# Kernel optimization log

Measured on AMD Instinct MI355X. Metric: run time of the kernel, lower is better.

Reference implementation:

```python
import jax, jax.numpy as jnp
import numpy as np
from jax import lax

EPS = 1e-5


def _dcn_core(value, offset, mask, offset_scale):
    # value: (B,H,W,G,D); offset: (B,H,W,G,K,2) as (dx,dy); mask: (B,H,W,G,K)
    # DCNv4: no softmax on mask; sampling loc = center + (kernel_grid + offset)*offset_scale
    B, H, W, G, D = value.shape
    K = mask.shape[-1]
    P = H * W
    kr = jnp.arange(3, dtype=value.dtype) - 1.0
    gy, gx = jnp.meshgrid(kr, kr, indexing="ij")  # 3x3 kernel grid
    gx = gx.reshape(1, 1, 1, 1, K)
    gy = gy.reshape(1, 1, 1, 1, K)
    bx = jnp.arange(W, dtype=value.dtype).reshape(1, 1, W, 1, 1)
    by = jnp.arange(H, dtype=value.dtype).reshape(1, H, 1, 1, 1)
    ix = bx + (gx + offset[..., 0]) * offset_scale  # (B,H,W,G,K) pixel-index coords
    iy = by + (gy + offset[..., 1]) * offset_scale

    tog = lambda a: a.transpose(0, 3, 1, 2, 4).reshape(B, G, P, K)
    ix, iy, m = tog(ix), tog(iy), tog(mask)
    vflat = value.transpose(0, 3, 1, 2, 4).reshape(B, G, P, D)

    x0 = jnp.floor(ix)
    y0 = jnp.floor(iy)
    tx = ix - x0
    ty = iy - y0
    out = jnp.zeros((B, G, P, D), value.dtype)
    # bilinear with zero padding (grid_sample padding_mode='zeros', align_corners=False)
    for dy, dx, wgt in ((0, 0, (1 - ty) * (1 - tx)), (0, 1, (1 - ty) * tx),
                        (1, 0, ty * (1 - tx)), (1, 1, ty * tx)):
        xc = x0 + dx
        yc = y0 + dy
        valid = ((xc >= 0) & (xc < W) & (yc >= 0) & (yc < H)).astype(value.dtype)
        lin = (jnp.clip(yc, 0, H - 1) * W + jnp.clip(xc, 0, W - 1)).astype(jnp.int32)
        v = jnp.take_along_axis(vflat, lin.reshape(B, G, P * K, 1), axis=2)
        v = v.reshape(B, G, P, K, D)
        out = out + jnp.einsum("bgpk,bgpkd->bgpd", wgt * m * valid, v)
    return out.transpose(0, 2, 1, 3).reshape(B, P, G * D)


def setup_inputs() -> dict:
    key = jax.random.key(0)
    ks = jax.random.split(key, 6)
    C = 64
    r = lambda k, shp, s: jax.random.normal(k, shp, jnp.float32) * s
    return {
        "x": r(ks[0], (8, C, 128, 128), 1.0),
        "vp_w": r(ks[1], (C, C), C ** -0.5),
        "vp_b": jnp.zeros((C,), jnp.float32),
        "dw_w": r(ks[2], (C, 1, 3, 3), 1.0 / 3.0),
        "dw_b": jnp.zeros((C,), jnp.float32),
        "om_w": r(ks[3], (56, C), 0.01),
        "om_b": jnp.zeros((56,), jnp.float32),
        "op_w": r(ks[4], (C, C), C ** -0.5),
        "op_b": jnp.zeros((C,), jnp.float32),
        "bn_g": jnp.ones((C // 2,), jnp.float32),
        "bn_b": jnp.zeros((C // 2,), jnp.float32),
        "bn_m": jnp.zeros((C // 2,), jnp.float32),
        "bn_v": jnp.ones((C // 2,), jnp.float32),
    }


def reference(x, vp_w, vp_b, dw_w, dw_b, om_w, om_b, op_w, op_b, bn_g, bn_b, bn_m, bn_v):
    B, C, H, W = x.shape
    G, K, OS = 2, 9, 2.0  # group = in_planes//out_planes = 2; 3x3 -> K=9
    seq = x.reshape(B, H * W, C)  # raw reshape exactly as the torch code
    # DCNv4 value_proj
    val = seq @ vp_w.T + vp_b
    value = val.reshape(B, H, W, G, C // G)
    # offset/mask branch: depthwise 3x3 conv on raw input, then linear
    xi = seq.reshape(B, H, W, C).transpose(0, 3, 1, 2)  # (B,C,H,W)
    dw = lax.conv_general_dilated(xi, dw_w, (1, 1), "SAME",
                                  dimension_numbers=("NCHW", "OIHW", "NCHW"),
                                  feature_group_count=C)
    dw = dw + dw_b[None, :, None, None]
    om = dw.transpose(0, 2, 3, 1) @ om_w.T + om_b  # (B,H,W,56)
    om = om[..., : G * K * 3].reshape(B, H, W, G, 3 * K)  # drop pad-to-8 tail
    offset = om[..., : 2 * K].reshape(B, H, W, G, K, 2)
    mask = om[..., 2 * K:]
    core = _dcn_core(value, offset, mask, OS)  # (B, HW, C)
    out = (core @ op_w.T + op_b).reshape(B, C, H, W)  # raw reshape, as in torch code
    z = 0.5 * (out[:, : C // 2] + out[:, C // 2:])  # chunk + average
    z = bn_g[:, None, None] * (z - bn_m[:, None, None]) * lax.rsqrt(bn_v + EPS)[:, None, None] + bn_b[:, None, None]
    return jnp.maximum(z, 0.0)
```

## Files before the change

kernel.cpp:

```cpp
#include <hip/hip_runtime.h>

#define B_ 8
#define H_ 128
#define W_ 128
#define P_ 16384
#define C_ 64
#define NQ (B_*P_)

typedef _Float16 fp16;
typedef _Float16 half2v __attribute__((ext_vector_type(2)));
typedef _Float16 half4v __attribute__((ext_vector_type(4)));
typedef _Float16 half8v __attribute__((ext_vector_type(8)));

static __device__ __forceinline__ void fma4s(float4& a, float s, const float4& v) {
  a.x += s * v.x; a.y += s * v.y; a.z += s * v.z; a.w += s * v.w;
}
static __device__ __forceinline__ void fma4e(float4& a, const float4& u, const float4& v) {
  a.x += u.x * v.x; a.y += u.y * v.y; a.z += u.z * v.z; a.w += u.w * v.w;
}
static __device__ __forceinline__ float4 h2f(half4v h) {
  return make_float4((float)h.x, (float)h.y, (float)h.z, (float)h.w);
}
static __device__ __forceinline__ half4v f2h(float4 a) {
  half4v hv;
  hv.x = (fp16)a.x; hv.y = (fp16)a.y; hv.z = (fp16)a.z; hv.w = (fp16)a.w;
  return hv;
}

__global__ __launch_bounds__(256) void gemm_val_kernel(
    const float* __restrict__ X, const float* __restrict__ W,
    const float* __restrict__ bias, fp16* __restrict__ val) {
  __shared__ __align__(16) float Xs[128][68];
  __shared__ __align__(16) float Ws[64][68];
  int tid = threadIdx.x;
  int bid = blockIdx.x;
  int logical = (bid & 7) * 128 + (bid >> 3);
  size_t row0 = (size_t)logical * 128;

#pragma unroll
  for (int i0 = 0; i0 < 8192; i0 += 1024) {
    int i = i0 + tid * 4;
    int r = i >> 6, k = i & 63;
    *(float4*)&Xs[r][k] = *(const float4*)(X + row0 * 64 + i);
  }
#pragma unroll
  for (int i0 = 0; i0 < 4096; i0 += 1024) {
    int i = i0 + tid * 4;
    int c = i >> 6, k = i & 63;
    float4 wv = *(const float4*)(W + i);
    Ws[k][c] = wv.x; Ws[k + 1][c] = wv.y; Ws[k + 2][c] = wv.z; Ws[k + 3][c] = wv.w;
  }
  __syncthreads();

  int ty = tid >> 4, tx = tid & 15;
  int c0 = tx * 4;
  float4 b4 = *(const float4*)(bias + c0);
  float4 acc[8];
#pragma unroll
  for (int rr = 0; rr < 8; ++rr) acc[rr] = b4;
#pragma unroll 4
  for (int k0 = 0; k0 < 64; k0 += 4) {
    float4 w0 = *(const float4*)&Ws[k0][c0];
    float4 w1 = *(const float4*)&Ws[k0 + 1][c0];
    float4 w2 = *(const float4*)&Ws[k0 + 2][c0];
    float4 w3 = *(const float4*)&Ws[k0 + 3][c0];
#pragma unroll
    for (int rr = 0; rr < 8; ++rr) {
      float4 xv = *(const float4*)&Xs[ty + rr * 16][k0];
      fma4s(acc[rr], xv.x, w0); fma4s(acc[rr], xv.y, w1);
      fma4s(acc[rr], xv.z, w2); fma4s(acc[rr], xv.w, w3);
    }
  }
#pragma unroll
  for (int rr = 0; rr < 8; ++rr) {
    int r = ty + rr * 16;
    *(half4v*)(val + (row0 + r) * 64 + c0) = f2h(acc[rr]);
  }
}

__global__ __launch_bounds__(256) void dwom_kernel(
    const float* __restrict__ X, const float* __restrict__ dw_w,
    const float* __restrict__ dw_b, const float* __restrict__ om_w,
    const float* __restrict__ om_b, fp16* __restrict__ OM) {
  __shared__ __align__(16) fp16 dws[64][76];
  __shared__ __align__(16) fp16 omwT[64][60];
  __shared__ __align__(16) float dwwT[9][68];
  __shared__ float dwbs[64];
  __shared__ float ombs[56];
  int tid = threadIdx.x;
  int bid = blockIdx.x;
  int logical = (bid & 7) * 256 + (bid >> 3);
  int b = logical >> 8;
  int lg = logical & 255;
  int q0 = b * 16384 + lg * 64;
  int h = lg >> 1;
  int w0 = (lg & 1) * 64;

  for (int i = tid; i < 3456; i += 256) omwT[i & 63][i >> 6] = (fp16)om_w[i];
  for (int i = tid; i < 576; i += 256) dwwT[i % 9][i / 9] = dw_w[i];
  if (tid < 64) dwbs[tid] = dw_b[tid];
  if (tid < 56) ombs[tid] = (tid < 54) ? om_b[tid] : 0.f;
  __syncthreads();

  {
    int cv = tid & 15;
    int wq = tid >> 4;
    int c0 = cv * 4;
    int wbase = w0 + wq * 4;
    const float* xb = X + (size_t)b * 1048576 + c0;
    const float* rp0 = xb + (size_t)(h - 1) * 8192;
    const float* rp1 = xb + (size_t)h * 8192;
    const float* rp2 = xb + (size_t)(h + 1) * 8192;
    bool v0 = (h > 0), v2 = (h < 127);
    float4 wt[9];
#pragma unroll
    for (int t = 0; t < 9; ++t) wt[t] = *(const float4*)&dwwT[t][c0];
    float4 dwb4 = *(const float4*)&dwbs[c0];
    const float4 z4 = make_float4(0.f, 0.f, 0.f, 0.f);
    bool vm = (wbase > 0);
    float4 cm0 = (vm && v0) ? *(const float4*)(rp0 + (wbase - 1) * 64) : z4;
    float4 cm1 = vm         ? *(const float4*)(rp1 + (wbase - 1) * 64) : z4;
    float4 cm2 = (vm && v2) ? *(const float4*)(rp2 + (wbase - 1) * 64) : z4;
    float4 cc0 = v0 ? *(const float4*)(rp0 + wbase * 64) : z4;
    float4 cc1 =      *(const float4*)(rp1 + wbase * 64);
    float4 cc2 = v2 ? *(const float4*)(rp2 + wbase * 64) : z4;
#pragma unroll
    for (int j = 0; j < 4; ++j) {
      int w = wbase + j;
      bool vn = (w < 127);
      float4 cn0 = (vn && v0) ? *(const float4*)(rp0 + (w + 1) * 64) : z4;
      float4 cn1 = vn         ? *(const float4*)(rp1 + (w + 1) * 64) : z4;
      float4 cn2 = (vn && v2) ? *(const float4*)(rp2 + (w + 1) * 64) : z4;
      float4 acc = dwb4;
      fma4e(acc, cm0, wt[0]); fma4e(acc, cc0, wt[1]); fma4e(acc, cn0, wt[2]);
      fma4e(acc, cm1, wt[3]); fma4e(acc, cc1, wt[4]); fma4e(acc, cn1, wt[5]);
      fma4e(acc, cm2, wt[6]); fma4e(acc, cc2, wt[7]); fma4e(acc, cn2, wt[8]);
      *(half4v*)&dws[wq * 4 + j][c0] = f2h(acc);
      cm0 = cc0; cm1 = cc1; cm2 = cc2;
      cc0 = cn0; cc1 = cn1; cc2 = cn2;
    }
  }
  __syncthreads();

  int ty = tid >> 4, tx = tid & 15;
  int o0 = tx * 4;
  if (o0 < 54) {
    float4 b4 = *(const float4*)&ombs[o0];
    float4 acc[4] = {b4, b4, b4, b4};
#pragma unroll 4
    for (int k0 = 0; k0 < 64; k0 += 4) {
      float4 w0 = h2f(*(const half4v*)&omwT[k0][o0]);
      float4 w1 = h2f(*(const half4v*)&omwT[k0 + 1][o0]);
      float4 w2 = h2f(*(const half4v*)&omwT[k0 + 2][o0]);
      float4 w3 = h2f(*(const half4v*)&omwT[k0 + 3][o0]);
#pragma unroll
      for (int rr = 0; rr < 4; ++rr) {
        float4 dv = h2f(*(const half4v*)&dws[ty * 4 + rr][k0]);
        fma4s(acc[rr], dv.x, w0); fma4s(acc[rr], dv.y, w1);
        fma4s(acc[rr], dv.z, w2); fma4s(acc[rr], dv.w, w3);
      }
    }
#pragma unroll
    for (int rr = 0; rr < 4; ++rr) {
      int r = ty * 4 + rr;
      size_t base = (size_t)(q0 + r) * 54 + o0;
      if (o0 <= 48) {
        *(half4v*)(OM + base) = f2h(acc[rr]);
      } else {
        half2v hv2;
        hv2.x = (fp16)acc[rr].x; hv2.y = (fp16)acc[rr].y;
        *(half2v*)(OM + base) = hv2;
      }
    }
  }
}

__global__ __launch_bounds__(256, 6) void gather_kernel(
    const fp16* __restrict__ val, const fp16* __restrict__ OM,
    fp16* __restrict__ core) {
  __shared__ __align__(16) float4 wtab[64 * 2 * 9];
  __shared__ int btab[64 * 2 * 9];
  int tid = threadIdx.x;
  int bid = blockIdx.x;
  int logical = (bid & 7) * 256 + (bid >> 3);
  int b = logical >> 8;
  int q0 = logical * 64;

  for (int i = tid; i < 1152; i += 256) {
    int row = i / 18;
    int rem = i - row * 18;
    int g = rem / 9;
    int k = rem - g * 9;
    int q = q0 + row;
    int p = q & 16383;
    int h = p >> 7, w = p & 127;
    const fp16* omq = OM + (size_t)q * 54 + g * 27;
    float ox = (float)omq[2 * k], oy = (float)omq[2 * k + 1];
    float m = (float)omq[18 + k];
    int kx = k - (k / 3) * 3, ky = k / 3;
    float ix = (float)w + ((float)kx - 1.0f + ox) * 2.0f;
    float iy = (float)h + ((float)ky - 1.0f + oy) * 2.0f;
    float x0f = floorf(ix), y0f = floorf(iy);
    float tx = ix - x0f, ty = iy - y0f;
    int x0 = (int)x0f, y0 = (int)y0f;
    int x1 = x0 + 1, y1 = y0 + 1;
    float vx0 = ((unsigned)x0 < 128u) ? 1.f : 0.f;
    float vx1 = ((unsigned)x1 < 128u) ? 1.f : 0.f;
    float vy0 = ((unsigned)y0 < 128u) ? 1.f : 0.f;
    float vy1 = ((unsigned)y1 < 128u) ? 1.f : 0.f;
    int xc0 = min(max(x0, 0), 127), xc1 = min(max(x1, 0), 127);
    int yc0 = min(max(y0, 0), 127), yc1 = min(max(y1, 0), 127);
    float4 w4;
    w4.x = (1.f - ty) * (1.f - tx) * m * vy0 * vx0;
    w4.y = (1.f - ty) * tx * m * vy0 * vx1;
    w4.z = ty * (1.f - tx) * m * vy1 * vx0;
    w4.w = ty * tx * m * vy1 * vx1;
    wtab[i] = w4;
    btab[i] = (yc0 * 128 + xc0) | ((xc1 - xc0) << 14) | ((yc1 - yc0) << 15);
  }
  __syncthreads();

  int lq = tid >> 4;
  int g = (tid >> 3) & 1;
  int dv = tid & 7;
  const fp16* vbase = val + ((size_t)b << 20) + g * 32 + dv * 4;
  fp16* cbase = core + (size_t)q0 * 64 + g * 32 + dv * 4;
  for (int t = 0; t < 4; ++t) {
    int row = lq + 16 * t;
    int base = (row * 2 + g) * 9;
    float4 acc = make_float4(0.f, 0.f, 0.f, 0.f);
#pragma unroll
    for (int k = 0; k < 9; ++k) {
      float4 w4 = wtab[base + k];
      int pk = btab[base + k];
      int lin00 = pk & 16383;
      int dxo = (pk >> 14) & 1;
      int lin10 = lin00 + ((pk >> 15) << 7);
      half4v v00 = *(const half4v*)(vbase + ((size_t)lin00 << 6));
      half4v v01 = *(const half4v*)(vbase + ((size_t)(lin00 + dxo) << 6));
      half4v v10 = *(const half4v*)(vbase + ((size_t)lin10 << 6));
      half4v v11 = *(const half4v*)(vbase + ((size_t)(lin10 + dxo) << 6));
      fma4s(acc, w4.x, h2f(v00));
      fma4s(acc, w4.y, h2f(v01));
      fma4s(acc, w4.z, h2f(v10));
      fma4s(acc, w4.w, h2f(v11));
    }
    *(half4v*)(cbase + ((size_t)row << 6)) = f2h(acc);
  }
}

__global__ __launch_bounds__(256) void gemmbn_kernel(
    const fp16* __restrict__ core, const float* __restrict__ op_w,
    const float* __restrict__ op_b, const float* __restrict__ bn_g,
    const float* __restrict__ bn_b, const float* __restrict__ bn_m,
    const float* __restrict__ bn_v, float* __restrict__ out) {
  __shared__ __align__(16) float Ws[64][68];
  __shared__ __align__(16) fp16 csL[64][72];
  __shared__ __align__(16) fp16 csH[64][72];
  int tid = threadIdx.x;
  int bid = blockIdx.x;
  int logical = (bid & 7) * 128 + (bid >> 3);
  int b = logical >> 7;
  int p0 = (logical & 127) * 64;
  size_t q0lo = (size_t)b * 16384 + p0;

#pragma unroll
  for (int i0 = 0; i0 < 4096; i0 += 1024) {
    int i = i0 + tid * 4;
    int c = i >> 6, k = i & 63;
    float4 wv = *(const float4*)(op_w + i);
    Ws[k][c] = wv.x; Ws[k + 1][c] = wv.y; Ws[k + 2][c] = wv.z; Ws[k + 3][c] = wv.w;
  }
#pragma unroll
  for (int j0 = 0; j0 < 512; j0 += 256) {
    int j = j0 + tid;
    int r = j >> 3;
    int cc = (j & 7) * 8;
    *(half8v*)&csL[r][cc] = *(const half8v*)(core + (q0lo + r) * 64 + cc);
    *(half8v*)&csH[r][cc] = *(const half8v*)(core + (q0lo + 8192 + r) * 64 + cc);
  }
  __syncthreads();

  int ty = tid >> 4, tx = tid & 15;
  int c0 = tx * 4;
  float4 accL[4], accH[4];
#pragma unroll
  for (int m = 0; m < 4; ++m) {
    accL[m] = make_float4(0.f, 0.f, 0.f, 0.f);
    accH[m] = make_float4(0.f, 0.f, 0.f, 0.f);
  }
#pragma unroll 2
  for (int k0 = 0; k0 < 64; k0 += 4) {
    float4 w0 = *(const float4*)&Ws[k0][c0];
    float4 w1 = *(const float4*)&Ws[k0 + 1][c0];
    float4 w2 = *(const float4*)&Ws[k0 + 2][c0];
    float4 w3 = *(const float4*)&Ws[k0 + 3][c0];
#pragma unroll
    for (int m = 0; m < 4; ++m) {
      int r = ty + 16 * m;
      float4 aL = h2f(*(const half4v*)&csL[r][k0]);
      float4 aH = h2f(*(const half4v*)&csH[r][k0]);
      fma4s(accL[m], aL.x, w0); fma4s(accL[m], aL.y, w1);
      fma4s(accL[m], aL.z, w2); fma4s(accL[m], aL.w, w3);
      fma4s(accH[m], aH.x, w0); fma4s(accH[m], aH.y, w1);
      fma4s(accH[m], aH.z, w2); fma4s(accH[m], aH.w, w3);
    }
  }
  float4 bias4 = *(const float4*)(op_b + c0);
#pragma unroll
  for (int m = 0; m < 4; ++m) {
    int r = ty + 16 * m;
    int f = (p0 + r) * 64 + c0;
    int c2 = f >> 14;
    float scale = bn_g[c2] * rsqrtf(bn_v[c2] + 1e-5f);
    float shift = bn_b[c2] - bn_m[c2] * scale;
    float4 z;
    z.x = fmaxf((0.5f * (accL[m].x + accH[m].x) + bias4.x) * scale + shift, 0.f);
    z.y = fmaxf((0.5f * (accL[m].y + accH[m].y) + bias4.y) * scale + shift, 0.f);
    z.z = fmaxf((0.5f * (accL[m].z + accH[m].z) + bias4.z) * scale + shift, 0.f);
    z.w = fmaxf((0.5f * (accL[m].w + accH[m].w) + bias4.w) * scale + shift, 0.f);
    *(float4*)(out + (size_t)b * 524288 + f) = z;
  }
}

extern "C" void kernel_launch(void* const* d_in, const int* in_sizes, int n_in,
                              void* d_out, int out_size, void* d_ws, size_t ws_size,
                              hipStream_t stream) {
  const float* x    = (const float*)d_in[0];
  const float* vp_w = (const float*)d_in[1];
  const float* vp_b = (const float*)d_in[2];
  const float* dw_w = (const float*)d_in[3];
  const float* dw_b = (const float*)d_in[4];
  const float* om_w = (const float*)d_in[5];
  const float* om_b = (const float*)d_in[6];
  const float* op_w = (const float*)d_in[7];
  const float* op_b = (const float*)d_in[8];
  const float* bn_g = (const float*)d_in[9];
  const float* bn_b = (const float*)d_in[10];
  const float* bn_m = (const float*)d_in[11];
  const float* bn_v = (const float*)d_in[12];

  fp16* val_h  = (fp16*)d_ws;
  fp16* core_h = (fp16*)((char*)d_ws + (16u << 20));
  fp16* om_h   = (fp16*)((char*)d_ws + (32u << 20));

  gemm_val_kernel<<<dim3(1024), dim3(256), 0, stream>>>(x, vp_w, vp_b, val_h);
  dwom_kernel<<<dim3(2048), dim3(256), 0, stream>>>(x, dw_w, dw_b, om_w, om_b, om_h);
  gather_kernel<<<dim3(2048), dim3(256), 0, stream>>>(val_h, om_h, core_h);
  gemmbn_kernel<<<dim3(1024), dim3(256), 0, stream>>>(
      core_h, op_w, op_b, bn_g, bn_b, bn_m, bn_v, (float*)d_out);
}
```

Baseline: 123.1 us.

## Move offset/mask linear from depthwise kernel into gather kernel via shared memory

Splits the depthwise conv into its own kernel, which writes the 64-channel fp16 dw output, and fuses the offset/mask linear projection into the gather kernel. The projection result now stays in shared memory instead of going through a global OM buffer. The bilinear weight table is stored as fp16 to reduce LDS use, and gather occupancy is lowered to 4 blocks per CU. The trade is a larger intermediate in HBM (64 channels instead of 54) and more LDS and work per gather block, in exchange for removing the OM global round trip. The fp16 weights also add rounding error.

```diff
diff --git a/kernel.cpp b/kernel.cpp
--- a/kernel.cpp
+++ b/kernel.cpp
@@ -78,15 +78,11 @@
   }
 }
 
-__global__ __launch_bounds__(256) void dwom_kernel(
+__global__ __launch_bounds__(256) void dw_kernel(
     const float* __restrict__ X, const float* __restrict__ dw_w,
-    const float* __restrict__ dw_b, const float* __restrict__ om_w,
-    const float* __restrict__ om_b, fp16* __restrict__ OM) {
-  __shared__ __align__(16) fp16 dws[64][76];
-  __shared__ __align__(16) fp16 omwT[64][60];
+    const float* __restrict__ dw_b, fp16* __restrict__ dws) {
   __shared__ __align__(16) float dwwT[9][68];
   __shared__ float dwbs[64];
-  __shared__ float ombs[56];
   int tid = threadIdx.x;
   int bid = blockIdx.x;
   int logical = (bid & 7) * 256 + (bid >> 3);
@@ -96,95 +92,108 @@
   int h = lg >> 1;
   int w0 = (lg & 1) * 64;
 
-  for (int i = tid; i < 3456; i += 256) omwT[i & 63][i >> 6] = (fp16)om_w[i];
   for (int i = tid; i < 576; i += 256) dwwT[i % 9][i / 9] = dw_w[i];
   if (tid < 64) dwbs[tid] = dw_b[tid];
-  if (tid < 56) ombs[tid] = (tid < 54) ? om_b[tid] : 0.f;
-  __syncthreads();
-
-  {
-    int cv = tid & 15;
-    int wq = tid >> 4;
-    int c0 = cv * 4;
-    int wbase = w0 + wq * 4;
-    const float* xb = X + (size_t)b * 1048576 + c0;
-    const float* rp0 = xb + (size_t)(h - 1) * 8192;
-    const float* rp1 = xb + (size_t)h * 8192;
-    const float* rp2 = xb + (size_t)(h + 1) * 8192;
-    bool v0 = (h > 0), v2 = (h < 127);
-    float4 wt[9];
-#pragma unroll
-    for (int t = 0; t < 9; ++t) wt[t] = *(const float4*)&dwwT[t][c0];
-    float4 dwb4 = *(const float4*)&dwbs[c0];
-    const float4 z4 = make_float4(0.f, 0.f, 0.f, 0.f);
-    bool vm = (wbase > 0);
-    float4 cm0 = (vm && v0) ? *(const float4*)(rp0 + (wbase - 1) * 64) : z4;
-    float4 cm1 = vm         ? *(const float4*)(rp1 + (wbase - 1) * 64) : z4;
-    float4 cm2 = (vm && v2) ? *(const float4*)(rp2 + (wbase - 1) * 64) : z4;
-    float4 cc0 = v0 ? *(const float4*)(rp0 + wbase * 64) : z4;
-    float4 cc1 =      *(const float4*)(rp1 + wbase * 64);
-    float4 cc2 = v2 ? *(const float4*)(rp2 + wbase * 64) : z4;
-#pragma unroll
-    for (int j = 0; j < 4; ++j) {
-      int w = wbase + j;
-      bool vn = (w < 127);
-      float4 cn0 = (vn && v0) ? *(const float4*)(rp0 + (w + 1) * 64) : z4;
-      float4 cn1 = vn         ? *(const float4*)(rp1 + (w + 1) * 64) : z4;
-      float4 cn2 = (vn && v2) ? *(const float4*)(rp2 + (w + 1) * 64) : z4;
-      float4 acc = dwb4;
-      fma4e(acc, cm0, wt[0]); fma4e(acc, cc0, wt[1]); fma4e(acc, cn0, wt[2]);
-      fma4e(acc, cm1, wt[3]); fma4e(acc, cc1, wt[4]); fma4e(acc, cn1, wt[5]);
-      fma4e(acc, cm2, wt[6]); fma4e(acc, cc2, wt[7]); fma4e(acc, cn2, wt[8]);
-      *(half4v*)&dws[wq * 4 + j][c0] = f2h(acc);
-      cm0 = cc0; cm1 = cc1; cm2 = cc2;
-      cc0 = cn0; cc1 = cn1; cc2 = cn2;
-    }
-  }
-  __syncthreads();
-
-  int ty = tid >> 4, tx = tid & 15;
-  int o0 = tx * 4;
-  if (o0 < 54) {
-    float4 b4 = *(const float4*)&ombs[o0];
-    float4 acc[4] = {b4, b4, b4, b4};
-#pragma unroll 4
-    for (int k0 = 0; k0 < 64; k0 += 4) {
-      float4 w0 = h2f(*(const half4v*)&omwT[k0][o0]);
-      float4 w1 = h2f(*(const half4v*)&omwT[k0 + 1][o0]);
-      float4 w2 = h2f(*(const half4v*)&omwT[k0 + 2][o0]);
-      float4 w3 = h2f(*(const half4v*)&omwT[k0 + 3][o0]);
-#pragma unroll
-      for (int rr = 0; rr < 4; ++rr) {
-        float4 dv = h2f(*(const half4v*)&dws[ty * 4 + rr][k0]);
-        fma4s(acc[rr], dv.x, w0); fma4s(acc[rr], dv.y, w1);
-        fma4s(acc[rr], dv.z, w2); fma4s(acc[rr], dv.w, w3);
-      }
-    }
-#pragma unroll
-    for (int rr = 0; rr < 4; ++rr) {
-      int r = ty * 4 + rr;
-      size_t base = (size_t)(q0 + r) * 54 + o0;
-      if (o0 <= 48) {
-        *(half4v*)(OM + base) = f2h(acc[rr]);
-      } else {
-        half2v hv2;
-        hv2.x = (fp16)acc[rr].x; hv2.y = (fp16)acc[rr].y;
-        *(half2v*)(OM + base) = hv2;
-      }
-    }
-  }
-}
-
-__global__ __launch_bounds__(256, 6) void gather_kernel(
-    const fp16* __restrict__ val, const fp16* __restrict__ OM,
+  __syncthreads();
+
+  int cv = tid & 15;
+  int wq = tid >> 4;
+  int c0 = cv * 4;
+  int wbase = w0 + wq * 4;
+  const float* xb = X + (size_t)b * 1048576 + c0;
+  const float* rp0 = xb + (size_t)(h - 1) * 8192;
+  const float* rp1 = xb + (size_t)h * 8192;
+  const float* rp2 = xb + (size_t)(h + 1) * 8192;
+  bool v0 = (h > 0), v2 = (h < 127);
+  float4 wt[9];
+#pragma unroll
+  for (int t = 0; t < 9; ++t) wt[t] = *(const float4*)&dwwT[t][c0];
+  float4 dwb4 = *(const float4*)&dwbs[c0];
+  const float4 z4 = make_float4(0.f, 0.f, 0.f, 0.f);
+  bool vm = (wbase > 0);
+  float4 cm0 = (vm && v0) ? *(const float4*)(rp0 + (wbase - 1) * 64) : z4;
+  float4 cm1 = vm         ? *(const float4*)(rp1 + (wbase - 1) * 64) : z4;
+  float4 cm2 = (vm && v2) ? *(const float4*)(rp2 + (wbase - 1) * 64) : z4;
+  float4 cc0 = v0 ? *(const float4*)(rp0 + wbase * 64) : z4;
+  float4 cc1 =      *(const float4*)(rp1 + wbase * 64);
+  float4 cc2 = v2 ? *(const float4*)(rp2 + wbase * 64) : z4;
+#pragma unroll
+  for (int j = 0; j < 4; ++j) {
+    int w = wbase + j;
+    bool vn = (w < 127);
+    float4 cn0 = (vn && v0) ? *(const float4*)(rp0 + (w + 1) * 64) : z4;
+    float4 cn1 = vn         ? *(const float4*)(rp1 + (w + 1) * 64) : z4;
+    float4 cn2 = (vn && v2) ? *(const float4*)(rp2 + (w + 1) * 64) : z4;
+    float4 acc = dwb4;
+    fma4e(acc, cm0, wt[0]); fma4e(acc, cc0, wt[1]); fma4e(acc, cn0, wt[2]);
+    fma4e(acc, cm1, wt[3]); fma4e(acc, cc1, wt[4]); fma4e(acc, cn1, wt[5]);
+    fma4e(acc, cm2, wt[6]); fma4e(acc, cc2, wt[7]); fma4e(acc, cn2, wt[8]);
+    *(half4v*)(dws + (size_t)(q0 + wq * 4 + j) * 64 + c0) = f2h(acc);
+    cm0 = cc0; cm1 = cc1; cm2 = cc2;
+    cc0 = cn0; cc1 = cn1; cc2 = cn2;
+  }
+}
+
+__global__ __launch_bounds__(256, 4) void gather_kernel(
+    const fp16* __restrict__ val, const fp16* __restrict__ dws,
+    const float* __restrict__ om_w, const float* __restrict__ om_b,
     fp16* __restrict__ core) {
-  __shared__ __align__(16) float4 wtab[64 * 2 * 9];
+  __shared__ __align__(16) fp16 dws_s[64][68];
+  __shared__ __align__(16) fp16 omwT[64][60];
+  __shared__ __align__(16) fp16 oms[64][56];
+  __shared__ __align__(16) half4v wtab[64 * 2 * 9];
   __shared__ int btab[64 * 2 * 9];
+  __shared__ float ombs[56];
   int tid = threadIdx.x;
   int bid = blockIdx.x;
   int logical = (bid & 7) * 256 + (bid >> 3);
   int b = logical >> 8;
   int q0 = logical * 64;
+
+#pragma unroll
+  for (int j0 = 0; j0 < 512; j0 += 256) {
+    int j = j0 + tid;
+    int r = j >> 3;
+    int cc = (j & 7) * 8;
+    *(half8v*)&dws_s[r][cc] = *(const half8v*)(dws + ((size_t)q0 + r) * 64 + cc);
+  }
+  for (int i = tid; i < 3456; i += 256) omwT[i & 63][i >> 6] = (fp16)om_w[i];
+  if (tid < 56) ombs[tid] = (tid < 54) ? om_b[tid] : 0.f;
+  __syncthreads();
+
+  {
+    int ty = tid >> 4, tx = tid & 15;
+    int o0 = tx * 4;
+    if (o0 < 54) {
+      float4 b4 = *(const float4*)&ombs[o0];
+      float4 acc[4] = {b4, b4, b4, b4};
+#pragma unroll 4
+      for (int k0 = 0; k0 < 64; k0 += 4) {
+        float4 w0 = h2f(*(const half4v*)&omwT[k0][o0]);
+        float4 w1 = h2f(*(const half4v*)&omwT[k0 + 1][o0]);
+        float4 w2 = h2f(*(const half4v*)&omwT[k0 + 2][o0]);
+        float4 w3 = h2f(*(const half4v*)&omwT[k0 + 3][o0]);
+#pragma unroll
+        for (int rr = 0; rr < 4; ++rr) {
+          float4 dv = h2f(*(const half4v*)&dws_s[ty * 4 + rr][k0]);
+          fma4s(acc[rr], dv.x, w0); fma4s(acc[rr], dv.y, w1);
+          fma4s(acc[rr], dv.z, w2); fma4s(acc[rr], dv.w, w3);
+        }
+      }
+#pragma unroll
+      for (int rr = 0; rr < 4; ++rr) {
+        int r = ty * 4 + rr;
+        if (o0 <= 48) {
+          *(half4v*)&oms[r][o0] = f2h(acc[rr]);
+        } else {
+          half2v hv2;
+          hv2.x = (fp16)acc[rr].x; hv2.y = (fp16)acc[rr].y;
+          *(half2v*)&oms[r][o0] = hv2;
+        }
+      }
+    }
+  }
+  __syncthreads();
 
   for (int i = tid; i < 1152; i += 256) {
     int row = i / 18;
@@ -194,9 +203,9 @@
     int q = q0 + row;
     int p = q & 16383;
     int h = p >> 7, w = p & 127;
-    const fp16* omq = OM + (size_t)q * 54 + g * 27;
-    float ox = (float)omq[2 * k], oy = (float)omq[2 * k + 1];
-    float m = (float)omq[18 + k];
+    float ox = (float)oms[row][g * 27 + 2 * k];
+    float oy = (float)oms[row][g * 27 + 2 * k + 1];
+    float m  = (float)oms[row][g * 27 + 18 + k];
     int kx = k - (k / 3) * 3, ky = k / 3;
     float ix = (float)w + ((float)kx - 1.0f + ox) * 2.0f;
     float iy = (float)h + ((float)ky - 1.0f + oy) * 2.0f;
@@ -215,7 +224,7 @@
     w4.y = (1.f - ty) * tx * m * vy0 * vx1;
     w4.z = ty * (1.f - tx) * m * vy1 * vx0;
     w4.w = ty * tx * m * vy1 * vx1;
-    wtab[i] = w4;
+    wtab[i] = f2h(w4);
     btab[i] = (yc0 * 128 + xc0) | ((xc1 - xc0) << 14) | ((yc1 - yc0) << 15);
   }
   __syncthreads();
@@ -231,7 +240,7 @@
     float4 acc = make_float4(0.f, 0.f, 0.f, 0.f);
 #pragma unroll
     for (int k = 0; k < 9; ++k) {
-      float4 w4 = wtab[base + k];
+      float4 w4 = h2f(wtab[base + k]);
       int pk = btab[base + k];
       int lin00 = pk & 16383;
       int dxo = (pk >> 14) & 1;
@@ -342,11 +351,11 @@
 
   fp16* val_h  = (fp16*)d_ws;
   fp16* core_h = (fp16*)((char*)d_ws + (16u << 20));
-  fp16* om_h   = (fp16*)((char*)d_ws + (32u << 20));
+  fp16* dws_h  = (fp16*)((char*)d_ws + (32u << 20));
 
   gemm_val_kernel<<<dim3(1024), dim3(256), 0, stream>>>(x, vp_w, vp_b, val_h);
-  dwom_kernel<<<dim3(2048), dim3(256), 0, stream>>>(x, dw_w, dw_b, om_w, om_b, om_h);
-  gather_kernel<<<dim3(2048), dim3(256), 0, stream>>>(val_h, om_h, core_h);
+  dw_kernel<<<dim3(2048), dim3(256), 0, stream>>>(x, dw_w, dw_b, dws_h);
+  gather_kernel<<<dim3(2048), dim3(256), 0, stream>>>(val_h, dws_h, om_w, om_b, core_h);
   gemmbn_kernel<<<dim3(1024), dim3(256), 0, stream>>>(
       core_h, op_w, op_b, bn_g, bn_b, bn_m, bn_v, (float*)d_out);
 }
```

After: 134.0 us. +8.9%, slower.
